# Optimization experiments

Hardware: AMD Instinct MI355X
Metric: run time of the kernel (lower is better)

The kernel has to match this reference:

```python
import jax, jax.numpy as jnp
import numpy as np

D, H, F, N, V, B, S, T = 512, 8, 2048, 2, 32000, 2, 1024, 1024


def _pe(seq_len, d):
    pos = np.arange(seq_len)[:, None].astype(np.float32)
    div = np.exp(np.arange(0, d, 2).astype(np.float32) * (-np.log(10000.0) / d))
    pe = np.zeros((seq_len, d), np.float32)
    pe[:, 0::2] = np.sin(pos * div)
    pe[:, 1::2] = np.cos(pos * div)
    return jnp.asarray(pe)


def _ln(x, g, b, eps=1e-6):
    # torch .var() default is unbiased (ddof=1)
    m = x.mean(-1, keepdims=True)
    v = jnp.sum((x - m) ** 2, -1, keepdims=True) / (x.shape[-1] - 1)
    return g * (x - m) / jnp.sqrt(v + eps) + b


def _mha(q, k, v, mask, w, b):
    # w: [4, D, D] (q,k,v,o); b: [4, D]
    Bq, Sq, Dm = q.shape
    Sk = k.shape[1]
    dk = Dm // H
    Q = (q @ w[0] + b[0]).reshape(Bq, Sq, H, dk).transpose(0, 2, 1, 3)
    K = (k @ w[1] + b[1]).reshape(Bq, Sk, H, dk).transpose(0, 2, 1, 3)
    Vv = (v @ w[2] + b[2]).reshape(Bq, Sk, H, dk).transpose(0, 2, 1, 3)
    s = jnp.einsum('bhqd,bhkd->bhqk', Q, K) / jnp.sqrt(jnp.float32(dk))
    s = jnp.where(mask == 0, jnp.float32(-1e9), s)
    a = jax.nn.softmax(s, axis=-1)
    o = jnp.einsum('bhqk,bhkd->bhqd', a, Vv).transpose(0, 2, 1, 3).reshape(Bq, Sq, Dm)
    return o @ w[3] + b[3]


def _ffn(x, w1, b1, w2, b2):
    return jax.nn.relu(x @ w1 + b1) @ w2 + b2


def _forward(src, tgt, src_mask, tgt_mask, p):
    (src_emb, tgt_emb, ea_w, ea_b, ef_w1, ef_b1, ef_w2, ef_b2, eln_g, eln_b, en_g, en_b,
     ds_w, ds_b, dc_w, dc_b, df_w1, df_b1, df_w2, df_b2, dln_g, dln_b, dn_g, dn_b, pw, pb) = p
    scale = jnp.sqrt(jnp.float32(D))
    # encoder
    x = src_emb[src] * scale + _pe(src.shape[1], D)
    for i in range(N):
        h = _ln(x, eln_g[i, 0], eln_b[i, 0])
        x = x + _mha(h, h, h, src_mask, ea_w[i], ea_b[i])
        h = _ln(x, eln_g[i, 1], eln_b[i, 1])
        x = x + _ffn(h, ef_w1[i], ef_b1[i], ef_w2[i], ef_b2[i])
    enc = _ln(x, en_g, en_b)
    # decoder
    y = tgt_emb[tgt] * scale + _pe(tgt.shape[1], D)
    for i in range(N):
        h = _ln(y, dln_g[i, 0], dln_b[i, 0])
        y = y + _mha(h, h, h, tgt_mask, ds_w[i], ds_b[i])
        h = _ln(y, dln_g[i, 1], dln_b[i, 1])
        y = y + _mha(h, enc, enc, src_mask, dc_w[i], dc_b[i])
        h = _ln(y, dln_g[i, 2], dln_b[i, 2])
        y = y + _ffn(h, df_w1[i], df_b1[i], df_w2[i], df_b2[i])
    y = _ln(y, dn_g, dn_b)
    return jax.nn.log_softmax(y @ pw + pb, axis=-1)


def setup_inputs() -> dict:
    key = jax.random.key(0)
    c = [0]
    def nk():
        c[0] += 1
        return jax.random.fold_in(key, c[0])
    def w(*s):
        return jax.random.normal(nk(), s, jnp.float32) * 0.02
    inp = {
        'src': jax.random.randint(nk(), (B, S), 0, V, jnp.int32),
        'tgt': jax.random.randint(nk(), (B, T), 0, V, jnp.int32),
        'src_mask': jnp.ones((B, 1, 1, S), jnp.int32),
        'tgt_mask': jnp.tril(jnp.ones((T, T), jnp.int32))[None, None],
        'src_emb': w(V, D), 'tgt_emb': w(V, D),
        'enc_attn_w': w(N, 4, D, D), 'enc_attn_b': jnp.zeros((N, 4, D), jnp.float32),
        'enc_ffn_w1': w(N, D, F), 'enc_ffn_b1': jnp.zeros((N, F), jnp.float32),
        'enc_ffn_w2': w(N, F, D), 'enc_ffn_b2': jnp.zeros((N, D), jnp.float32),
        'enc_ln_g': jnp.ones((N, 2, D), jnp.float32), 'enc_ln_b': jnp.zeros((N, 2, D), jnp.float32),
        'enc_norm_g': jnp.ones((D,), jnp.float32), 'enc_norm_b': jnp.zeros((D,), jnp.float32),
        'dec_self_w': w(N, 4, D, D), 'dec_self_b': jnp.zeros((N, 4, D), jnp.float32),
        'dec_cross_w': w(N, 4, D, D), 'dec_cross_b': jnp.zeros((N, 4, D), jnp.float32),
        'dec_ffn_w1': w(N, D, F), 'dec_ffn_b1': jnp.zeros((N, F), jnp.float32),
        'dec_ffn_w2': w(N, F, D), 'dec_ffn_b2': jnp.zeros((N, D), jnp.float32),
        'dec_ln_g': jnp.ones((N, 3, D), jnp.float32), 'dec_ln_b': jnp.zeros((N, 3, D), jnp.float32),
        'dec_norm_g': jnp.ones((D,), jnp.float32), 'dec_norm_b': jnp.zeros((D,), jnp.float32),
        'proj_w': w(D, V), 'proj_b': jnp.zeros((V,), jnp.float32),
    }
    return inp


def reference(src, tgt, src_mask, tgt_mask, src_emb, tgt_emb, enc_attn_w, enc_attn_b,
              enc_ffn_w1, enc_ffn_b1, enc_ffn_w2, enc_ffn_b2, enc_ln_g, enc_ln_b,
              enc_norm_g, enc_norm_b, dec_self_w, dec_self_b, dec_cross_w, dec_cross_b,
              dec_ffn_w1, dec_ffn_b1, dec_ffn_w2, dec_ffn_b2, dec_ln_g, dec_ln_b,
              dec_norm_g, dec_norm_b, proj_w, proj_b):
    p = (src_emb, tgt_emb, enc_attn_w, enc_attn_b, enc_ffn_w1, enc_ffn_b1, enc_ffn_w2,
         enc_ffn_b2, enc_ln_g, enc_ln_b, enc_norm_g, enc_norm_b, dec_self_w, dec_self_b,
         dec_cross_w, dec_cross_b, dec_ffn_w1, dec_ffn_b1, dec_ffn_w2, dec_ffn_b2,
         dec_ln_g, dec_ln_b, dec_norm_g, dec_norm_b, proj_w, proj_b)
    return _forward(src, tgt, src_mask, tgt_mask, p)
```

## Files before the change

kernel.cpp:

```cpp
#include <hip/hip_runtime.h>
#include <hip/hip_bf16.h>
#include <math.h>

using bf16 = __hip_bfloat16;
typedef float f32x4 __attribute__((ext_vector_type(4)));
typedef short short8 __attribute__((ext_vector_type(8)));

constexpr int kD = 512, kH = 8, kDk = 64, kF = 2048, kV = 32000;
constexpr int kB = 2, kS = 1024, kM = 2048, kBH = 16;

enum { ST_F32 = 0, ST_BF16, ST_QKV };

__device__ __forceinline__ void gload_lds16(const void* g, void* l) {
  __builtin_amdgcn_global_load_lds(
      (const __attribute__((address_space(1))) void*)g,
      (__attribute__((address_space(3))) void*)l, 16, 0, 0);
}

__device__ __forceinline__ float bfu2f(short u) {
  union { unsigned int i; float f; } c;
  c.i = ((unsigned int)(unsigned short)u) << 16;
  return c.f;
}

template <int BM, int BN, int STM, bool BIAS, bool RELU, bool RES, int NBUF, bool XSWZ, bool ASEL>
__launch_bounds__(256)
__global__ void k_gemm(const bf16* __restrict__ A, int lda, long long Az,
                       const bf16* __restrict__ Bt, int ldb, long long Bz,
                       void* __restrict__ Cv, int ldc, long long Cz,
                       int K, float alpha,
                       const float* __restrict__ bias,
                       const float* __restrict__ res,
                       const bf16* __restrict__ A2) {
  static_assert(NBUF == 1 || (BM == 64 && BN == 64), "pipeline path sized for 64x64");
  constexpr int FM = BM / 32, FN = BN / 32;
  __shared__ __attribute__((aligned(16))) bf16 As[NBUF][BM * 64];
  __shared__ __attribute__((aligned(16))) bf16 Bs[NBUF][BN * 64];
  const int tid = threadIdx.x;
  const int w = tid >> 6, lane = tid & 63;
  int bx = blockIdx.x, by = blockIdx.y;
  if constexpr (XSWZ) {
    const int nx = gridDim.x, ny = gridDim.y;
    const int lin = by * nx + bx;
    const int cpx = (nx * ny) >> 3;
    const int s = (lin & 7) * cpx + (lin >> 3);
    bx = s / ny;
    by = s - bx * ny;
  }
  const int bm = by * BM, bn = bx * BN;
  const int z = blockIdx.z;
  if constexpr (ASEL) { if (bn >= 512) A = A2; }
  A += (long long)z * Az;
  Bt += (long long)z * Bz;
  const int l15 = lane & 15, lhi = lane >> 4;
  const int wr = (w >> 1) * (BM / 2), wc = (w & 1) * (BN / 2);
  f32x4 acc[FM][FN] = {};
  const int nkt = K >> 6;

  auto stage = [&](int kt, int nb) {
#pragma unroll
    for (int it = 0; it < BM / 32; ++it) {
      int chunk = (it * 4 + w) * 64 + lane;
      int row = chunk >> 3, col = (chunk & 7) << 3;
      gload_lds16(A + (size_t)(bm + row) * lda + kt * 64 + col, As[nb] + (it * 4 + w) * 512);
    }
#pragma unroll
    for (int it = 0; it < BN / 32; ++it) {
      int chunk = (it * 4 + w) * 64 + lane;
      int row = chunk >> 3, col = (chunk & 7) << 3;
      gload_lds16(Bt + (size_t)(bn + row) * ldb + kt * 64 + col, Bs[nb] + (it * 4 + w) * 512);
    }
  };
  auto compute = [&](int cb) {
#pragma unroll
    for (int kk = 0; kk < 2; ++kk) {
      short8 af[FM], bf[FN];
#pragma unroll
      for (int i = 0; i < FM; ++i)
        af[i] = *(const short8*)(As[cb] + (wr + i * 16 + l15) * 64 + kk * 32 + lhi * 8);
#pragma unroll
      for (int j = 0; j < FN; ++j)
        bf[j] = *(const short8*)(Bs[cb] + (wc + j * 16 + l15) * 64 + kk * 32 + lhi * 8);
#pragma unroll
      for (int i = 0; i < FM; ++i)
#pragma unroll
        for (int j = 0; j < FN; ++j)
          acc[i][j] = __builtin_amdgcn_mfma_f32_16x16x32_bf16(af[i], bf[j], acc[i][j], 0, 0, 0);
    }
  };

  if constexpr (NBUF == 3) {
    stage(0, 0);
    stage(1, 1);
    stage(2, 2);
    asm volatile("s_waitcnt vmcnt(8)" ::: "memory");
    __builtin_amdgcn_s_barrier();
    __builtin_amdgcn_sched_barrier(0);
    int cur = 0;
    for (int kt = 0; kt < nkt; ++kt) {
      compute(cur);
      asm volatile("s_waitcnt lgkmcnt(0)" ::: "memory");
      __builtin_amdgcn_sched_barrier(0);
      if (kt + 1 < nkt) {
        __builtin_amdgcn_s_barrier();
        if (kt + 3 < nkt) {
          stage(kt + 3, cur);
          asm volatile("s_waitcnt vmcnt(8)" ::: "memory");
        } else {
          asm volatile("s_waitcnt vmcnt(0)" ::: "memory");
        }
        __builtin_amdgcn_s_barrier();
        __builtin_amdgcn_sched_barrier(0);
      }
      cur = (cur == 2) ? 0 : cur + 1;
    }
  } else {
    for (int kt = 0; kt < nkt; ++kt) {
      stage(kt, 0);
      __syncthreads();
      compute(0);
      __syncthreads();
    }
  }

#pragma unroll
  for (int i = 0; i < FM; ++i) {
#pragma unroll
    for (int j = 0; j < FN; ++j) {
#pragma unroll
      for (int r = 0; r < 4; ++r) {
        int m = bm + wr + i * 16 + lhi * 4 + r;
        int n = bn + wc + j * 16 + l15;
        float val = acc[i][j][r] * alpha;
        if constexpr (BIAS) val += bias[n];
        if constexpr (RELU) val = fmaxf(val, 0.f);
        if constexpr (RES) val += res[(size_t)m * ldc + n];
        if constexpr (STM == ST_F32) {
          ((float*)Cv)[(size_t)z * Cz + (size_t)m * ldc + n] = val;
        } else if constexpr (STM == ST_BF16) {
          ((bf16*)Cv)[(size_t)z * Cz + (size_t)m * ldc + n] = __float2bfloat16(val);
        } else if constexpr (STM == ST_QKV) {
          int seg = n >> 9, nn = n & 511;
          int b_ = m >> 10, s_ = m & 1023, h_ = nn >> 6, d_ = nn & 63;
          size_t idx = (seg < 2)
              ? (((size_t)(b_ * kH + h_) << 10) + s_) * kDk + d_
              : ((size_t)(b_ * kH + h_) * kDk + d_) * kS + s_;
          ((bf16*)Cv)[(size_t)seg * 1048576 + idx] = __float2bfloat16(val);
        }
      }
    }
  }
}

__global__ __launch_bounds__(512, 1) void k_proj256(const bf16* __restrict__ A,
                                                    const bf16* __restrict__ Bt,
                                                    bf16* __restrict__ C,
                                                    const float* __restrict__ bias) {
  __shared__ __attribute__((aligned(16))) bf16 As[4][256 * 32];
  __shared__ __attribute__((aligned(16))) bf16 Bs[4][256 * 32];
  const int tid = threadIdx.x, w = tid >> 6, lane = tid & 63;
  const int l15 = lane & 15, lhi = lane >> 4;
  const int lin = blockIdx.y * 125 + blockIdx.x;
  const int s = (lin & 7) * 125 + (lin >> 3);
  const int bx = s >> 3, by = s & 7;
  const int bm = by * 256, bn = bx * 256;
  const int wr = (w >> 2) * 128, wc = (w & 3) * 64;
  const int rowq = tid >> 2, chk = tid & 3;
  const int swz = (chk ^ ((rowq >> 1) & 3)) << 3;
  const bf16* Asrc0 = A + (size_t)(bm + rowq) * kD + swz;
  const bf16* Asrc1 = A + (size_t)(bm + 128 + rowq) * kD + swz;
  const bf16* Bsrc0 = Bt + (size_t)(bn + rowq) * kD + swz;
  const bf16* Bsrc1 = Bt + (size_t)(bn + 128 + rowq) * kD + swz;
  const int ldsoff = w * 1024;

  auto stage = [&](int kt) {
    const int b = kt & 3;
    const int ko = kt * 32;
    gload_lds16(Asrc0 + ko, (char*)As[b] + ldsoff);
    gload_lds16(Asrc1 + ko, (char*)As[b] + 8192 + ldsoff);
    gload_lds16(Bsrc0 + ko, (char*)Bs[b] + ldsoff);
    gload_lds16(Bsrc1 + ko, (char*)Bs[b] + 8192 + ldsoff);
  };

  const int ra = wr + l15, rb = wc + l15;
  const int abase = ra * 64 + ((lhi ^ ((ra >> 1) & 3)) << 4);
  const int bbase = rb * 64 + ((lhi ^ ((rb >> 1) & 3)) << 4);

  f32x4 acc[8][4] = {};
  stage(0); stage(1); stage(2);
  for (int kt = 0; kt < 16; ++kt) {
    if (kt + 2 < 16)      asm volatile("s_waitcnt vmcnt(8)" ::: "memory");
    else if (kt + 1 < 16) asm volatile("s_waitcnt vmcnt(4)" ::: "memory");
    else                  asm volatile("s_waitcnt vmcnt(0)" ::: "memory");
    __builtin_amdgcn_s_barrier();
    __builtin_amdgcn_sched_barrier(0);
    if (kt + 3 < 16) stage(kt + 3);
    const int b = kt & 3;
    short8 af[8], bf[4];
#pragma unroll
    for (int i = 0; i < 8; ++i)
      af[i] = *(const short8*)((const char*)As[b] + abase + i * 1024);
#pragma unroll
    for (int j = 0; j < 4; ++j)
      bf[j] = *(const short8*)((const char*)Bs[b] + bbase + j * 1024);
#pragma unroll
    for (int i = 0; i < 8; ++i)
#pragma unroll
      for (int j = 0; j < 4; ++j)
        acc[i][j] = __builtin_amdgcn_mfma_f32_16x16x32_bf16(af[i], bf[j], acc[i][j], 0, 0, 0);
    asm volatile("s_waitcnt lgkmcnt(0)" ::: "memory");
    __builtin_amdgcn_sched_barrier(0);
  }
#pragma unroll
  for (int i = 0; i < 8; ++i)
#pragma unroll
    for (int j = 0; j < 4; ++j)
#pragma unroll
      for (int r = 0; r < 4; ++r) {
        int m = bm + wr + i * 16 + lhi * 4 + r;
        int n = bn + wc + j * 16 + l15;
        C[(size_t)m * kV + n] = __float2bfloat16(acc[i][j][r] + bias[n]);
      }
}

template <bool CAUSAL>
__launch_bounds__(256)
__global__ void k_fattn(const bf16* __restrict__ Q, const bf16* __restrict__ K,
                        const bf16* __restrict__ Vt, bf16* __restrict__ O) {
  __shared__ __attribute__((aligned(16))) bf16 Ks[3][4096];
  __shared__ __attribute__((aligned(16))) bf16 Vs[3][4096];
  __shared__ __attribute__((aligned(16))) bf16 Ps[4][1024];
  const int tid = threadIdx.x, w = tid >> 6, lane = tid & 63;
  const int l15 = lane & 15, lhi = lane >> 4;
  const int q0 = blockIdx.x * 64, bh = blockIdx.y;
  const int qw = q0 + w * 16;
  const bf16* Qp = Q + (((size_t)(bh << 10)) + qw + l15) * kDk;
  short8 aq[2];
  aq[0] = *(const short8*)(Qp + lhi * 8);
  aq[1] = *(const short8*)(Qp + 32 + lhi * 8);
  const int srow = w * 8 + (lane >> 3);
  const int sc = (lane & 7) ^ (srow & 7);
  const bf16* Ksrc = K + (((size_t)(bh << 10)) + srow) * kDk + sc * 8;
  const bf16* Vsrc = Vt + ((size_t)bh * kDk + srow) * kS + sc * 8;
  const int nt = CAUSAL ? (q0 >> 6) + 1 : (kS >> 6);

  auto stage = [&](int t, int nb) {
    int kv0 = t << 6;
    gload_lds16(Ksrc + (size_t)kv0 * kDk, Ks[nb] + w * 512);
    gload_lds16(Ksrc + (size_t)(kv0 + 32) * kDk, Ks[nb] + 2048 + w * 512);
    gload_lds16(Vsrc + kv0, Vs[nb] + w * 512);
    gload_lds16(Vsrc + kv0 + 32 * kS, Vs[nb] + 2048 + w * 512);
  };

  float m_[4], l_[4];
#pragma unroll
  for (int r = 0; r < 4; ++r) { m_[r] = -1e30f; l_[r] = 0.f; }
  f32x4 ao[4] = {};

  stage(0, 0);
  if (nt > 2) {
    stage(1, 1);
    stage(2, 2);
    asm volatile("s_waitcnt vmcnt(8)" ::: "memory");
  } else if (nt > 1) {
    stage(1, 1);
    asm volatile("s_waitcnt vmcnt(4)" ::: "memory");
  } else {
    asm volatile("s_waitcnt vmcnt(0)" ::: "memory");
  }
  __builtin_amdgcn_s_barrier();
  __builtin_amdgcn_sched_barrier(0);

  int cur = 0;
  for (int t = 0; t < nt; ++t) {
    f32x4 as[4] = {};
#pragma unroll
    for (int kk = 0; kk < 2; ++kk) {
      short8 bk[4];
#pragma unroll
      for (int nf = 0; nf < 4; ++nf) {
        int row = nf * 16 + l15;
        int c = (4 * kk + lhi) ^ (row & 7);
        bk[nf] = *(const short8*)(Ks[cur] + row * 64 + c * 8);
      }
#pragma unroll
      for (int nf = 0; nf < 4; ++nf)
        as[nf] = __builtin_amdgcn_mfma_f32_16x16x32_bf16(aq[kk], bk[nf], as[nf], 0, 0, 0);
    }
    float s[4][4];
#pragma unroll
    for (int nf = 0; nf < 4; ++nf)
#pragma unroll
      for (int r = 0; r < 4; ++r) {
        float v = as[nf][r] * 0.125f;
        if (CAUSAL && t == nt - 1) {
          int col = (t << 6) + nf * 16 + l15;
          int row = qw + lhi * 4 + r;
          if (col > row) v = -1e30f;
        }
        s[nf][r] = v;
      }
    float mn[4], scl[4], rsum[4];
#pragma unroll
    for (int r = 0; r < 4; ++r) {
      float mx = fmaxf(fmaxf(s[0][r], s[1][r]), fmaxf(s[2][r], s[3][r]));
      mx = fmaxf(mx, __shfl_xor(mx, 1));
      mx = fmaxf(mx, __shfl_xor(mx, 2));
      mx = fmaxf(mx, __shfl_xor(mx, 4));
      mx = fmaxf(mx, __shfl_xor(mx, 8));
      mn[r] = fmaxf(m_[r], mx);
      scl[r] = __expf(m_[r] - mn[r]);
      rsum[r] = 0.f;
    }
#pragma unroll
    for (int nf = 0; nf < 4; ++nf)
#pragma unroll
      for (int r = 0; r < 4; ++r) {
        float p = __expf(s[nf][r] - mn[r]);
        rsum[r] += p;
        int pr = lhi * 4 + r;
        int c = (2 * nf + (l15 >> 3)) ^ (pr & 7);
        Ps[w][pr * 64 + c * 8 + (l15 & 7)] = __float2bfloat16(p);
      }
#pragma unroll
    for (int r = 0; r < 4; ++r) {
      float su = rsum[r];
      su += __shfl_xor(su, 1);
      su += __shfl_xor(su, 2);
      su += __shfl_xor(su, 4);
      su += __shfl_xor(su, 8);
      l_[r] = l_[r] * scl[r] + su;
      m_[r] = mn[r];
    }
#pragma unroll
    for (int nf = 0; nf < 4; ++nf)
#pragma unroll
      for (int r = 0; r < 4; ++r) ao[nf][r] *= scl[r];
    asm volatile("s_waitcnt lgkmcnt(0)" ::: "memory");
    __builtin_amdgcn_sched_barrier(0);
#pragma unroll
    for (int kk = 0; kk < 2; ++kk) {
      short8 pa = *(const short8*)(Ps[w] + l15 * 64 + (((4 * kk + lhi) ^ (l15 & 7)) * 8));
      short8 bv[4];
#pragma unroll
      for (int nf = 0; nf < 4; ++nf) {
        int row = nf * 16 + l15;
        int c = (4 * kk + lhi) ^ (row & 7);
        bv[nf] = *(const short8*)(Vs[cur] + row * 64 + c * 8);
      }
#pragma unroll
      for (int nf = 0; nf < 4; ++nf)
        ao[nf] = __builtin_amdgcn_mfma_f32_16x16x32_bf16(pa, bv[nf], ao[nf], 0, 0, 0);
    }
    asm volatile("s_waitcnt lgkmcnt(0)" ::: "memory");
    __builtin_amdgcn_sched_barrier(0);
    if (t + 1 < nt) {
      __builtin_amdgcn_s_barrier();
      if (t + 3 < nt) {
        stage(t + 3, cur);
        asm volatile("s_waitcnt vmcnt(8)" ::: "memory");
      } else {
        asm volatile("s_waitcnt vmcnt(0)" ::: "memory");
      }
      __builtin_amdgcn_s_barrier();
      __builtin_amdgcn_sched_barrier(0);
    }
    cur = (cur == 2) ? 0 : cur + 1;
  }
  const int b_ = bh >> 3, h_ = bh & 7;
  float inv[4];
#pragma unroll
  for (int r = 0; r < 4; ++r) inv[r] = 1.f / l_[r];
#pragma unroll
  for (int nf = 0; nf < 4; ++nf)
#pragma unroll
    for (int r = 0; r < 4; ++r) {
      int q = qw + lhi * 4 + r;
      O[((size_t)(b_ * kS + q)) * kD + h_ * kDk + nf * 16 + l15] =
          __float2bfloat16(ao[nf][r] * inv[r]);
    }
}

struct TJobs {
  const float* src[8];
  bf16* dst[8];
  int K[8], N[8];
  int ofs[9];
};

__global__ void k_transpose_all(TJobs J) {
  __shared__ float t[32][33];
  const int tb = blockIdx.x;
  int j = 0;
#pragma unroll
  for (int i = 1; i < 8; ++i) j += (tb >= J.ofs[i]) ? 1 : 0;
  const int K = J.K[j], N = J.N[j];
  const int tn = N >> 5, tk = K >> 5;
  int r = tb - J.ofs[j];
  const int z = r / (tn * tk);
  r -= z * tn * tk;
  const int k0 = (r / tn) << 5, n0 = (r % tn) << 5;
  const float* Wp = J.src[j] + (size_t)z * K * N;
  bf16* WTp = J.dst[j] + (size_t)z * K * N;
  const int tx = threadIdx.x, ty = threadIdx.y;
#pragma unroll
  for (int rr = 0; rr < 32; rr += 8) t[ty + rr][tx] = Wp[(size_t)(k0 + ty + rr) * N + n0 + tx];
  __syncthreads();
#pragma unroll
  for (int rr = 0; rr < 32; rr += 8)
    WTp[(size_t)(n0 + ty + rr) * K + k0 + tx] = __float2bfloat16(t[tx][ty + rr]);
}

__global__ void k_embed2(const int* __restrict__ src, const int* __restrict__ tgt,
                         const float* __restrict__ se, const float* __restrict__ te,
                         float* __restrict__ xe, float* __restrict__ xd) {
  const int m = blockIdx.x, which = blockIdx.y;
  const int* tok = which ? tgt : src;
  const float* emb = which ? te : se;
  float* x = which ? xd : xe;
  int s = m & (kS - 1);
  const float* e = emb + (size_t)tok[m] * kD;
  float* xp = x + (size_t)m * kD;
  for (int d = threadIdx.x; d < kD; d += 256) {
    int i = d >> 1;
    float freq = __expf(-(float)(2 * i) * (9.210340371976184f / 512.0f));
    float ang = (float)s * freq;
    float pe = (d & 1) ? cosf(ang) : sinf(ang);
    xp[d] = e[d] * 22.62741699796952f + pe;
  }
}

__global__ void k_ln(const float* __restrict__ x, const float* __restrict__ g,
                     const float* __restrict__ b, bf16* __restrict__ out) {
  int w = threadIdx.x >> 6, lane = threadIdx.x & 63;
  int row = blockIdx.x * 4 + w;
  const float* xp = x + (size_t)row * kD;
  float v[8];
  float sum = 0.f;
#pragma unroll
  for (int i = 0; i < 8; ++i) { v[i] = xp[lane + i * 64]; sum += v[i]; }
#pragma unroll
  for (int o = 32; o; o >>= 1) sum += __shfl_xor(sum, o);
  float mean = sum * (1.f / 512.f);
  float sq = 0.f;
#pragma unroll
  for (int i = 0; i < 8; ++i) { float d = v[i] - mean; sq += d * d; }
#pragma unroll
  for (int o = 32; o; o >>= 1) sq += __shfl_xor(sq, o);
  float inv = rsqrtf(sq * (1.f / 511.f) + 1e-6f);
  bf16* op = out + (size_t)row * kD;
#pragma unroll
  for (int i = 0; i < 8; ++i) {
    int d = lane + i * 64;
    op[d] = __float2bfloat16(g[d] * (v[i] - mean) * inv + b[d]);
  }
}

__global__ __launch_bounds__(640, 2) void k_lsm_bf(const bf16* __restrict__ L,
                                                   float* __restrict__ y) {
  const bf16* row = L + (size_t)blockIdx.x * kV;
  float* orow = y + (size_t)blockIdx.x * kV;
  const int t = threadIdx.x;
  const bool extra = t < 160;
  float v[56];
  float sum = 0.f;
#pragma unroll
  for (int i = 0; i < 6; ++i) {
    short8 s = *(const short8*)(row + (t + i * 640) * 8);
#pragma unroll
    for (int e = 0; e < 8; ++e) {
      float f = bfu2f(s[e]);
      v[i * 8 + e] = f;
      sum += __expf(f);
    }
  }
  if (extra) {
    short8 s = *(const short8*)(row + (3840 + t) * 8);
#pragma unroll
    for (int e = 0; e < 8; ++e) {
      float f = bfu2f(s[e]);
      v[48 + e] = f;
      sum += __expf(f);
    }
  }
#pragma unroll
  for (int o = 32; o; o >>= 1) sum += __shfl_xor(sum, o);
  __shared__ float red2[10];
  const int w = t >> 6, lane = t & 63;
  if (lane == 0) red2[w] = sum;
  __syncthreads();
  sum = 0.f;
#pragma unroll
  for (int i = 0; i < 10; ++i) sum += red2[i];
  const float sh = logf(sum);
#pragma unroll
  for (int i = 0; i < 6; ++i)
#pragma unroll
    for (int e = 0; e < 8; ++e) orow[(t + i * 640) * 8 + e] = v[i * 8 + e] - sh;
  if (extra)
#pragma unroll
    for (int e = 0; e < 8; ++e) orow[(3840 + t) * 8 + e] = v[48 + e] - sh;
}

extern "C" void kernel_launch(void* const* d_in, const int* in_sizes, int n_in,
                              void* d_out, int out_size, void* d_ws, size_t ws_size,
                              hipStream_t stream) {
  (void)in_sizes; (void)n_in; (void)out_size;
  if (ws_size < (size_t)212 * 1024 * 1024) return;

  const int* src = (const int*)d_in[0];
  const int* tgt = (const int*)d_in[1];
  const float* src_emb   = (const float*)d_in[4];
  const float* tgt_emb   = (const float*)d_in[5];
  const float* enc_attn_w = (const float*)d_in[6];
  const float* enc_attn_b = (const float*)d_in[7];
  const float* enc_ffn_w1 = (const float*)d_in[8];
  const float* enc_ffn_b1 = (const float*)d_in[9];
  const float* enc_ffn_w2 = (const float*)d_in[10];
  const float* enc_ffn_b2 = (const float*)d_in[11];
  const float* enc_ln_g  = (const float*)d_in[12];
  const float* enc_ln_b  = (const float*)d_in[13];
  const float* enc_norm_g = (const float*)d_in[14];
  const float* enc_norm_b = (const float*)d_in[15];
  const float* dec_self_w = (const float*)d_in[16];
  const float* dec_self_b = (const float*)d_in[17];
  const float* dec_cross_w = (const float*)d_in[18];
  const float* dec_cross_b = (const float*)d_in[19];
  const float* dec_ffn_w1 = (const float*)d_in[20];
  const float* dec_ffn_b1 = (const float*)d_in[21];
  const float* dec_ffn_w2 = (const float*)d_in[22];
  const float* dec_ffn_b2 = (const float*)d_in[23];
  const float* dec_ln_g  = (const float*)d_in[24];
  const float* dec_ln_b  = (const float*)d_in[25];
  const float* dec_norm_g = (const float*)d_in[26];
  const float* dec_norm_b = (const float*)d_in[27];
  const float* proj_w    = (const float*)d_in[28];
  const float* proj_b    = (const float*)d_in[29];

  char* ws = (char*)d_ws;
  auto MB = [](size_t x) { return x << 20; };
  bf16* enc_attn_wt  = (bf16*)(ws + MB(0));
  bf16* dec_self_wt  = (bf16*)(ws + MB(4));
  bf16* dec_cross_wt = (bf16*)(ws + MB(8));
  bf16* enc_f1t = (bf16*)(ws + MB(12));
  bf16* enc_f2t = (bf16*)(ws + MB(16));
  bf16* dec_f1t = (bf16*)(ws + MB(20));
  bf16* dec_f2t = (bf16*)(ws + MB(24));
  bf16* proj_wt = (bf16*)(ws + MB(28));
  float* x_enc  = (float*)(ws + MB(60));
  float* x_dec  = (float*)(ws + MB(64));
  bf16* hbuf    = (bf16*)(ws + MB(68));
  bf16* enc_bf  = (bf16*)(ws + MB(70));
  bf16* Qb      = (bf16*)(ws + MB(72));
  bf16* attn_o  = (bf16*)(ws + MB(78));
  bf16* logits  = (bf16*)(ws + MB(80));
  bf16* ffn_mid = (bf16*)d_out;

  TJobs tj;
  int acc = 0;
  auto setj = [&](int j, const float* s, bf16* d, int K, int N, int z) {
    tj.src[j] = s; tj.dst[j] = d; tj.K[j] = K; tj.N[j] = N; tj.ofs[j] = acc;
    acc += (K >> 5) * (N >> 5) * z;
  };
  setj(0, enc_attn_w, enc_attn_wt, 512, 512, 8);
  setj(1, dec_self_w, dec_self_wt, 512, 512, 8);
  setj(2, dec_cross_w, dec_cross_wt, 512, 512, 8);
  setj(3, enc_ffn_w1, enc_f1t, 512, 2048, 2);
  setj(4, enc_ffn_w2, enc_f2t, 2048, 512, 2);
  setj(5, dec_ffn_w1, dec_f1t, 512, 2048, 2);
  setj(6, dec_ffn_w2, dec_f2t, 2048, 512, 2);
  setj(7, proj_w, proj_wt, 512, 32000, 1);
  tj.ofs[8] = acc;
  k_transpose_all<<<acc, dim3(32, 8), 0, stream>>>(tj);

  k_embed2<<<dim3(kM, 2), 256, 0, stream>>>(src, tgt, src_emb, tgt_emb, x_enc, x_dec);

  auto LN = [&](const float* x, const float* g, const float* b, bf16* out) {
    k_ln<<<kM / 4, 256, 0, stream>>>(x, g, b, out);
  };
  auto out_proj = [&](const bf16* wt, const float* bias, float* xio) {
    k_gemm<64, 64, ST_F32, true, false, true, 3, false, false><<<dim3(8, 32, 1), 256, 0, stream>>>(
        attn_o, 512, 0, wt + 3 * 262144, 512, 0, xio, 512, 0, 512, 1.f, bias + 3 * 512, xio, nullptr);
  };
  auto self_attn = [&](const bf16* wt, const float* bias, bool causal, float* xio) {
    k_gemm<64, 64, ST_QKV, true, false, false, 3, false, false><<<dim3(24, 32, 1), 256, 0, stream>>>(
        hbuf, 512, 0, wt, 512, 0, Qb, 0, 0, 512, 1.f, bias, nullptr, nullptr);
    if (causal) k_fattn<true><<<dim3(16, kBH), 256, 0, stream>>>(Qb, Qb + 1048576, Qb + 2097152, attn_o);
    else        k_fattn<false><<<dim3(16, kBH), 256, 0, stream>>>(Qb, Qb + 1048576, Qb + 2097152, attn_o);
    out_proj(wt, bias, xio);
  };
  auto cross_attn = [&](const bf16* wt, const float* bias, float* xio) {
    k_gemm<64, 64, ST_QKV, true, false, false, 3, false, true><<<dim3(24, 32, 1), 256, 0, stream>>>(
        hbuf, 512, 0, wt, 512, 0, Qb, 0, 0, 512, 1.f, bias, nullptr, enc_bf);
    k_fattn<false><<<dim3(16, kBH), 256, 0, stream>>>(Qb, Qb + 1048576, Qb + 2097152, attn_o);
    out_proj(wt, bias, xio);
  };
  auto ffn_block = [&](float* xio, const bf16* w1t, const float* b1, const bf16* w2t,
                       const float* b2, const float* g, const float* bl) {
    LN(xio, g, bl, hbuf);
    k_gemm<64, 64, ST_BF16, true, true, false, 3, false, false><<<dim3(32, 32, 1), 256, 0, stream>>>(
        hbuf, 512, 0, w1t, 512, 0, ffn_mid, kF, 0, 512, 1.f, b1, nullptr, nullptr);
    k_gemm<64, 64, ST_F32, true, false, true, 3, false, false><<<dim3(8, 32, 1), 256, 0, stream>>>(
        ffn_mid, 2048, 0, w2t, 2048, 0, xio, 512, 0, 2048, 1.f, b2, xio, nullptr);
  };

  for (int i = 0; i < 2; ++i) {
    LN(x_enc, enc_ln_g + i * 1024, enc_ln_b + i * 1024, hbuf);
    self_attn(enc_attn_wt + (size_t)i * 1048576, enc_attn_b + i * 2048, false, x_enc);
    ffn_block(x_enc, enc_f1t + (size_t)i * 1048576, enc_ffn_b1 + i * 2048,
              enc_f2t + (size_t)i * 1048576, enc_ffn_b2 + i * 512,
              enc_ln_g + i * 1024 + 512, enc_ln_b + i * 1024 + 512);
  }
  LN(x_enc, enc_norm_g, enc_norm_b, enc_bf);

  for (int i = 0; i < 2; ++i) {
    LN(x_dec, dec_ln_g + i * 1536, dec_ln_b + i * 1536, hbuf);
    self_attn(dec_self_wt + (size_t)i * 1048576, dec_self_b + i * 2048, true, x_dec);
    LN(x_dec, dec_ln_g + i * 1536 + 512, dec_ln_b + i * 1536 + 512, hbuf);
    cross_attn(dec_cross_wt + (size_t)i * 1048576, dec_cross_b + i * 2048, x_dec);
    ffn_block(x_dec, dec_f1t + (size_t)i * 1048576, dec_ffn_b1 + i * 2048,
              dec_f2t + (size_t)i * 1048576, dec_ffn_b2 + i * 512,
              dec_ln_g + i * 1536 + 1024, dec_ln_b + i * 1536 + 1024);
  }
  LN(x_dec, dec_norm_g, dec_norm_b, hbuf);

  k_proj256<<<dim3(125, 8), 512, 0, stream>>>(hbuf, proj_wt, logits, proj_b);
  k_lsm_bf<<<kM, 640, 0, stream>>>(logits, (float*)d_out);
}
```

Measured before the change: 726.8 us.

## Fuse encoder/decoder layer kernels into a persistent megakernel with grid barriers

Replaces the sequence of many small kernel launches (transpose, embed, layernorm, QKV GEMM, attention, out-proj, FFN GEMMs) with one persistent 256-block kernel. Phases are separated by a software grid barrier built on atomics, and each block loops over virtual tiles. The aim is to remove launch overhead and inter-kernel gaps between dozens of short kernels. In exchange, occupancy is fixed at one 256-thread block per CU, some phases such as attention (256 tiles) or FFN1 (1024 tiles) may balance poorly, and each grid barrier adds its own spin-wait cost.

```diff
diff --git a/kernel.cpp b/kernel.cpp
--- a/kernel.cpp
+++ b/kernel.cpp
@@ -8,6 +8,7 @@
 
 constexpr int kD = 512, kH = 8, kDk = 64, kF = 2048, kV = 32000;
 constexpr int kB = 2, kS = 1024, kM = 2048, kBH = 16;
+constexpr unsigned kGrid = 256;
 
 enum { ST_F32 = 0, ST_BF16, ST_QKV };
 
@@ -23,122 +24,204 @@
   return c.f;
 }
 
-template <int BM, int BN, int STM, bool BIAS, bool RELU, bool RES, int NBUF, bool XSWZ, bool ASEL>
-__launch_bounds__(256)
-__global__ void k_gemm(const bf16* __restrict__ A, int lda, long long Az,
-                       const bf16* __restrict__ Bt, int ldb, long long Bz,
-                       void* __restrict__ Cv, int ldc, long long Cz,
-                       int K, float alpha,
-                       const float* __restrict__ bias,
-                       const float* __restrict__ res,
-                       const bf16* __restrict__ A2) {
-  static_assert(NBUF == 1 || (BM == 64 && BN == 64), "pipeline path sized for 64x64");
-  constexpr int FM = BM / 32, FN = BN / 32;
-  __shared__ __attribute__((aligned(16))) bf16 As[NBUF][BM * 64];
-  __shared__ __attribute__((aligned(16))) bf16 Bs[NBUF][BN * 64];
-  const int tid = threadIdx.x;
-  const int w = tid >> 6, lane = tid & 63;
-  int bx = blockIdx.x, by = blockIdx.y;
-  if constexpr (XSWZ) {
-    const int nx = gridDim.x, ny = gridDim.y;
-    const int lin = by * nx + bx;
-    const int cpx = (nx * ny) >> 3;
-    const int s = (lin & 7) * cpx + (lin >> 3);
-    bx = s / ny;
-    by = s - bx * ny;
-  }
-  const int bm = by * BM, bn = bx * BN;
-  const int z = blockIdx.z;
-  if constexpr (ASEL) { if (bn >= 512) A = A2; }
-  A += (long long)z * Az;
-  Bt += (long long)z * Bz;
+__device__ __forceinline__ void gbar(unsigned* bar, unsigned* gen) {
+  __threadfence();
+  __syncthreads();
+  if (threadIdx.x == 0) {
+    unsigned g = __hip_atomic_load(gen, __ATOMIC_RELAXED, __HIP_MEMORY_SCOPE_AGENT);
+    unsigned v = __hip_atomic_fetch_add(bar, 1u, __ATOMIC_ACQ_REL, __HIP_MEMORY_SCOPE_AGENT);
+    if (v == kGrid - 1u) {
+      __hip_atomic_store(bar, 0u, __ATOMIC_RELAXED, __HIP_MEMORY_SCOPE_AGENT);
+      __hip_atomic_store(gen, g + 1u, __ATOMIC_RELEASE, __HIP_MEMORY_SCOPE_AGENT);
+    } else {
+      while (__hip_atomic_load(gen, __ATOMIC_ACQUIRE, __HIP_MEMORY_SCOPE_AGENT) == g)
+        __builtin_amdgcn_s_sleep(2);
+    }
+  }
+  __syncthreads();
+}
+
+struct TJobs {
+  const float* src[8];
+  bf16* dst[8];
+  int K[8], N[8];
+  int ofs[9];
+};
+
+struct MegaArgs {
+  const int* src; const int* tgt;
+  const float* src_emb; const float* tgt_emb;
+  float* x_enc; float* x_dec;
+  TJobs tj; int ntile;
+  unsigned *bar, *gen;
+  bf16 *hbuf, *enc_bf, *Qb, *attn_o, *ffn_mid;
+  const bf16 *enc_attn_wt, *dec_self_wt, *dec_cross_wt;
+  const bf16 *enc_f1t, *enc_f2t, *dec_f1t, *dec_f2t;
+  const float *enc_attn_b, *enc_ffn_b1, *enc_ffn_b2, *enc_ln_g, *enc_ln_b;
+  const float *enc_norm_g, *enc_norm_b;
+  const float *dec_self_b, *dec_cross_b, *dec_ffn_b1, *dec_ffn_b2;
+  const float *dec_ln_g, *dec_ln_b, *dec_norm_g, *dec_norm_b;
+};
+
+
+__device__ __forceinline__ void transpose_tile(char* smemc, int tb, const TJobs& J) {
+  float (*t)[33] = (float (*)[33])smemc;
+  int j = 0;
+#pragma unroll
+  for (int i = 1; i < 8; ++i) j += (tb >= J.ofs[i]) ? 1 : 0;
+  const int K = J.K[j], N = J.N[j];
+  const int tn = N >> 5, tk = K >> 5;
+  int r = tb - J.ofs[j];
+  const int z = r / (tn * tk);
+  r -= z * tn * tk;
+  const int k0 = (r / tn) << 5, n0 = (r % tn) << 5;
+  const float* Wp = J.src[j] + (size_t)z * K * N;
+  bf16* WTp = J.dst[j] + (size_t)z * K * N;
+  const int tx = threadIdx.x & 31, ty = threadIdx.x >> 5;
+#pragma unroll
+  for (int rr = 0; rr < 32; rr += 8) t[ty + rr][tx] = Wp[(size_t)(k0 + ty + rr) * N + n0 + tx];
+  __syncthreads();
+#pragma unroll
+  for (int rr = 0; rr < 32; rr += 8)
+    WTp[(size_t)(n0 + ty + rr) * K + k0 + tx] = __float2bfloat16(t[tx][ty + rr]);
+  __syncthreads();
+}
+
+__device__ __forceinline__ void embed_row(int vb, const MegaArgs& a) {
+  const int m = vb & (kM - 1), which = vb >> 11;
+  const int* tok = which ? a.tgt : a.src;
+  const float* emb = which ? a.tgt_emb : a.src_emb;
+  float* x = which ? a.x_dec : a.x_enc;
+  int s = m & (kS - 1);
+  const float* e = emb + (size_t)tok[m] * kD;
+  float* xp = x + (size_t)m * kD;
+  for (int d = threadIdx.x; d < kD; d += 256) {
+    int i = d >> 1;
+    float freq = __expf(-(float)(2 * i) * (9.210340371976184f / 512.0f));
+    float ang = (float)s * freq;
+    float pe = (d & 1) ? cosf(ang) : sinf(ang);
+    xp[d] = e[d] * 22.62741699796952f + pe;
+  }
+}
+
+__device__ __forceinline__ void ln4(int vb, const float* __restrict__ x,
+                                    const float* __restrict__ g,
+                                    const float* __restrict__ b,
+                                    bf16* __restrict__ out) {
+  int w = threadIdx.x >> 6, lane = threadIdx.x & 63;
+  int row = vb * 4 + w;
+  const float* xp = x + (size_t)row * kD;
+  float v[8];
+  float sum = 0.f;
+#pragma unroll
+  for (int i = 0; i < 8; ++i) { v[i] = xp[lane + i * 64]; sum += v[i]; }
+#pragma unroll
+  for (int o = 32; o; o >>= 1) sum += __shfl_xor(sum, o);
+  float mean = sum * (1.f / 512.f);
+  float sq = 0.f;
+#pragma unroll
+  for (int i = 0; i < 8; ++i) { float d = v[i] - mean; sq += d * d; }
+#pragma unroll
+  for (int o = 32; o; o >>= 1) sq += __shfl_xor(sq, o);
+  float inv = rsqrtf(sq * (1.f / 511.f) + 1e-6f);
+  bf16* op = out + (size_t)row * kD;
+#pragma unroll
+  for (int i = 0; i < 8; ++i) {
+    int d = lane + i * 64;
+    op[d] = __float2bfloat16(g[d] * (v[i] - mean) * inv + b[d]);
+  }
+}
+
+template <int STM, bool BIAS, bool RELU, bool RES>
+__device__ __forceinline__ void gemm64_tile(
+    bf16* AsB, bf16* BsB, int bm, int bn,
+    const bf16* __restrict__ A, int lda,
+    const bf16* __restrict__ Bt, int ldb,
+    void* __restrict__ Cv, int ldc, int K,
+    const float* __restrict__ bias, const float* __restrict__ res) {
+  const int tid = threadIdx.x, w = tid >> 6, lane = tid & 63;
   const int l15 = lane & 15, lhi = lane >> 4;
-  const int wr = (w >> 1) * (BM / 2), wc = (w & 1) * (BN / 2);
-  f32x4 acc[FM][FN] = {};
+  const int wr = (w >> 1) * 32, wc = (w & 1) * 32;
+  f32x4 acc[2][2] = {};
   const int nkt = K >> 6;
 
   auto stage = [&](int kt, int nb) {
-#pragma unroll
-    for (int it = 0; it < BM / 32; ++it) {
+    bf16* As = AsB + nb * 4096;
+    bf16* Bs = BsB + nb * 4096;
+#pragma unroll
+    for (int it = 0; it < 2; ++it) {
       int chunk = (it * 4 + w) * 64 + lane;
       int row = chunk >> 3, col = (chunk & 7) << 3;
-      gload_lds16(A + (size_t)(bm + row) * lda + kt * 64 + col, As[nb] + (it * 4 + w) * 512);
-    }
-#pragma unroll
-    for (int it = 0; it < BN / 32; ++it) {
+      gload_lds16(A + (size_t)(bm + row) * lda + kt * 64 + col, As + (it * 4 + w) * 512);
+    }
+#pragma unroll
+    for (int it = 0; it < 2; ++it) {
       int chunk = (it * 4 + w) * 64 + lane;
       int row = chunk >> 3, col = (chunk & 7) << 3;
-      gload_lds16(Bt + (size_t)(bn + row) * ldb + kt * 64 + col, Bs[nb] + (it * 4 + w) * 512);
+      gload_lds16(Bt + (size_t)(bn + row) * ldb + kt * 64 + col, Bs + (it * 4 + w) * 512);
     }
   };
   auto compute = [&](int cb) {
+    bf16* As = AsB + cb * 4096;
+    bf16* Bs = BsB + cb * 4096;
 #pragma unroll
     for (int kk = 0; kk < 2; ++kk) {
-      short8 af[FM], bf[FN];
-#pragma unroll
-      for (int i = 0; i < FM; ++i)
-        af[i] = *(const short8*)(As[cb] + (wr + i * 16 + l15) * 64 + kk * 32 + lhi * 8);
-#pragma unroll
-      for (int j = 0; j < FN; ++j)
-        bf[j] = *(const short8*)(Bs[cb] + (wc + j * 16 + l15) * 64 + kk * 32 + lhi * 8);
-#pragma unroll
-      for (int i = 0; i < FM; ++i)
-#pragma unroll
-        for (int j = 0; j < FN; ++j)
+      short8 af[2], bf[2];
+#pragma unroll
+      for (int i = 0; i < 2; ++i)
+        af[i] = *(const short8*)(As + (wr + i * 16 + l15) * 64 + kk * 32 + lhi * 8);
+#pragma unroll
+      for (int j = 0; j < 2; ++j)
+        bf[j] = *(const short8*)(Bs + (wc + j * 16 + l15) * 64 + kk * 32 + lhi * 8);
+#pragma unroll
+      for (int i = 0; i < 2; ++i)
+#pragma unroll
+        for (int j = 0; j < 2; ++j)
           acc[i][j] = __builtin_amdgcn_mfma_f32_16x16x32_bf16(af[i], bf[j], acc[i][j], 0, 0, 0);
     }
   };
 
-  if constexpr (NBUF == 3) {
-    stage(0, 0);
-    stage(1, 1);
-    stage(2, 2);
-    asm volatile("s_waitcnt vmcnt(8)" ::: "memory");
-    __builtin_amdgcn_s_barrier();
+  stage(0, 0); stage(1, 1); stage(2, 2);
+  asm volatile("s_waitcnt vmcnt(8)" ::: "memory");
+  __builtin_amdgcn_s_barrier();
+  __builtin_amdgcn_sched_barrier(0);
+  int cur = 0;
+  for (int kt = 0; kt < nkt; ++kt) {
+    compute(cur);
+    asm volatile("s_waitcnt lgkmcnt(0)" ::: "memory");
     __builtin_amdgcn_sched_barrier(0);
-    int cur = 0;
-    for (int kt = 0; kt < nkt; ++kt) {
-      compute(cur);
-      asm volatile("s_waitcnt lgkmcnt(0)" ::: "memory");
+    if (kt + 1 < nkt) {
+      __builtin_amdgcn_s_barrier();
+      if (kt + 3 < nkt) {
+        stage(kt + 3, cur);
+        asm volatile("s_waitcnt vmcnt(8)" ::: "memory");
+      } else {
+        asm volatile("s_waitcnt vmcnt(0)" ::: "memory");
+      }
+      __builtin_amdgcn_s_barrier();
       __builtin_amdgcn_sched_barrier(0);
-      if (kt + 1 < nkt) {
-        __builtin_amdgcn_s_barrier();
-        if (kt + 3 < nkt) {
-          stage(kt + 3, cur);
-          asm volatile("s_waitcnt vmcnt(8)" ::: "memory");
-        } else {
-          asm volatile("s_waitcnt vmcnt(0)" ::: "memory");
-        }
-        __builtin_amdgcn_s_barrier();
-        __builtin_amdgcn_sched_barrier(0);
-      }
-      cur = (cur == 2) ? 0 : cur + 1;
-    }
-  } else {
-    for (int kt = 0; kt < nkt; ++kt) {
-      stage(kt, 0);
-      __syncthreads();
-      compute(0);
-      __syncthreads();
-    }
-  }
-
-#pragma unroll
-  for (int i = 0; i < FM; ++i) {
-#pragma unroll
-    for (int j = 0; j < FN; ++j) {
+    }
+    cur = (cur == 2) ? 0 : cur + 1;
+  }
+  __builtin_amdgcn_s_barrier();
+  __builtin_amdgcn_sched_barrier(0);
+
+#pragma unroll
+  for (int i = 0; i < 2; ++i) {
+#pragma unroll
+    for (int j = 0; j < 2; ++j) {
 #pragma unroll
       for (int r = 0; r < 4; ++r) {
         int m = bm + wr + i * 16 + lhi * 4 + r;
         int n = bn + wc + j * 16 + l15;
-        float val = acc[i][j][r] * alpha;
+        float val = acc[i][j][r];
         if constexpr (BIAS) val += bias[n];
         if constexpr (RELU) val = fmaxf(val, 0.f);
         if constexpr (RES) val += res[(size_t)m * ldc + n];
         if constexpr (STM == ST_F32) {
-          ((float*)Cv)[(size_t)z * Cz + (size_t)m * ldc + n] = val;
+          ((float*)Cv)[(size_t)m * ldc + n] = val;
         } else if constexpr (STM == ST_BF16) {
-          ((bf16*)Cv)[(size_t)z * Cz + (size_t)m * ldc + n] = __float2bfloat16(val);
+          ((bf16*)Cv)[(size_t)m * ldc + n] = __float2bfloat16(val);
         } else if constexpr (STM == ST_QKV) {
           int seg = n >> 9, nn = n & 511;
           int b_ = m >> 10, s_ = m & 1023, h_ = nn >> 6, d_ = nn & 63;
@@ -150,6 +233,255 @@
       }
     }
   }
+}
+
+template <bool CAUSAL>
+__device__ __forceinline__ void fattn_tile(bf16* Ks, bf16* Vs, bf16* Ps,
+                                           int qi, int bh,
+                                           const bf16* __restrict__ Q,
+                                           const bf16* __restrict__ K,
+                                           const bf16* __restrict__ Vt,
+                                           bf16* __restrict__ O) {
+  const int tid = threadIdx.x, w = tid >> 6, lane = tid & 63;
+  const int l15 = lane & 15, lhi = lane >> 4;
+  const int q0 = qi * 64;
+  const int qw = q0 + w * 16;
+  const bf16* Qp = Q + (((size_t)(bh << 10)) + qw + l15) * kDk;
+  short8 aq[2];
+  aq[0] = *(const short8*)(Qp + lhi * 8);
+  aq[1] = *(const short8*)(Qp + 32 + lhi * 8);
+  const int srow = w * 8 + (lane >> 3);
+  const int sc = (lane & 7) ^ (srow & 7);
+  const bf16* Ksrc = K + (((size_t)(bh << 10)) + srow) * kDk + sc * 8;
+  const bf16* Vsrc = Vt + ((size_t)bh * kDk + srow) * kS + sc * 8;
+  const int nt = CAUSAL ? (q0 >> 6) + 1 : (kS >> 6);
+
+  auto stage = [&](int t, int nb) {
+    int kv0 = t << 6;
+    gload_lds16(Ksrc + (size_t)kv0 * kDk, Ks + nb * 4096 + w * 512);
+    gload_lds16(Ksrc + (size_t)(kv0 + 32) * kDk, Ks + nb * 4096 + 2048 + w * 512);
+    gload_lds16(Vsrc + kv0, Vs + nb * 4096 + w * 512);
+    gload_lds16(Vsrc + kv0 + 32 * kS, Vs + nb * 4096 + 2048 + w * 512);
+  };
+
+  float m_[4], l_[4];
+#pragma unroll
+  for (int r = 0; r < 4; ++r) { m_[r] = -1e30f; l_[r] = 0.f; }
+  f32x4 ao[4] = {};
+
+  stage(0, 0);
+  if (nt > 2) {
+    stage(1, 1);
+    stage(2, 2);
+    asm volatile("s_waitcnt vmcnt(8)" ::: "memory");
+  } else if (nt > 1) {
+    stage(1, 1);
+    asm volatile("s_waitcnt vmcnt(4)" ::: "memory");
+  } else {
+    asm volatile("s_waitcnt vmcnt(0)" ::: "memory");
+  }
+  __builtin_amdgcn_s_barrier();
+  __builtin_amdgcn_sched_barrier(0);
+
+  int cur = 0;
+  for (int t = 0; t < nt; ++t) {
+    f32x4 as[4] = {};
+#pragma unroll
+    for (int kk = 0; kk < 2; ++kk) {
+      short8 bk[4];
+#pragma unroll
+      for (int nf = 0; nf < 4; ++nf) {
+        int row = nf * 16 + l15;
+        int c = (4 * kk + lhi) ^ (row & 7);
+        bk[nf] = *(const short8*)(Ks + cur * 4096 + row * 64 + c * 8);
+      }
+#pragma unroll
+      for (int nf = 0; nf < 4; ++nf)
+        as[nf] = __builtin_amdgcn_mfma_f32_16x16x32_bf16(aq[kk], bk[nf], as[nf], 0, 0, 0);
+    }
+    float s[4][4];
+#pragma unroll
+    for (int nf = 0; nf < 4; ++nf)
+#pragma unroll
+      for (int r = 0; r < 4; ++r) {
+        float v = as[nf][r] * 0.125f;
+        if (CAUSAL && t == nt - 1) {
+          int col = (t << 6) + nf * 16 + l15;
+          int row = qw + lhi * 4 + r;
+          if (col > row) v = -1e30f;
+        }
+        s[nf][r] = v;
+      }
+    float mn[4], scl[4], rsum[4];
+#pragma unroll
+    for (int r = 0; r < 4; ++r) {
+      float mx = fmaxf(fmaxf(s[0][r], s[1][r]), fmaxf(s[2][r], s[3][r]));
+      mx = fmaxf(mx, __shfl_xor(mx, 1));
+      mx = fmaxf(mx, __shfl_xor(mx, 2));
+      mx = fmaxf(mx, __shfl_xor(mx, 4));
+      mx = fmaxf(mx, __shfl_xor(mx, 8));
+      mn[r] = fmaxf(m_[r], mx);
+      scl[r] = __expf(m_[r] - mn[r]);
+      rsum[r] = 0.f;
+    }
+#pragma unroll
+    for (int nf = 0; nf < 4; ++nf)
+#pragma unroll
+      for (int r = 0; r < 4; ++r) {
+        float p = __expf(s[nf][r] - mn[r]);
+        rsum[r] += p;
+        int pr = lhi * 4 + r;
+        int c = (2 * nf + (l15 >> 3)) ^ (pr & 7);
+        Ps[w * 1024 + pr * 64 + c * 8 + (l15 & 7)] = __float2bfloat16(p);
+      }
+#pragma unroll
+    for (int r = 0; r < 4; ++r) {
+      float su = rsum[r];
+      su += __shfl_xor(su, 1);
+      su += __shfl_xor(su, 2);
+      su += __shfl_xor(su, 4);
+      su += __shfl_xor(su, 8);
+      l_[r] = l_[r] * scl[r] + su;
+      m_[r] = mn[r];
+    }
+#pragma unroll
+    for (int nf = 0; nf < 4; ++nf)
+#pragma unroll
+      for (int r = 0; r < 4; ++r) ao[nf][r] *= scl[r];
+    asm volatile("s_waitcnt lgkmcnt(0)" ::: "memory");
+    __builtin_amdgcn_sched_barrier(0);
+#pragma unroll
+    for (int kk = 0; kk < 2; ++kk) {
+      short8 pa = *(const short8*)(Ps + w * 1024 + l15 * 64 + (((4 * kk + lhi) ^ (l15 & 7)) * 8));
+      short8 bv[4];
+#pragma unroll
+      for (int nf = 0; nf < 4; ++nf) {
+        int row = nf * 16 + l15;
+        int c = (4 * kk + lhi) ^ (row & 7);
+        bv[nf] = *(const short8*)(Vs + cur * 4096 + row * 64 + c * 8);
+      }
+#pragma unroll
+      for (int nf = 0; nf < 4; ++nf)
+        ao[nf] = __builtin_amdgcn_mfma_f32_16x16x32_bf16(pa, bv[nf], ao[nf], 0, 0, 0);
+    }
+    asm volatile("s_waitcnt lgkmcnt(0)" ::: "memory");
+    __builtin_amdgcn_sched_barrier(0);
+    if (t + 1 < nt) {
+      __builtin_amdgcn_s_barrier();
+      if (t + 3 < nt) {
+        stage(t + 3, cur);
+        asm volatile("s_waitcnt vmcnt(8)" ::: "memory");
+      } else {
+        asm volatile("s_waitcnt vmcnt(0)" ::: "memory");
+      }
+      __builtin_amdgcn_s_barrier();
+      __builtin_amdgcn_sched_barrier(0);
+    }
+    cur = (cur == 2) ? 0 : cur + 1;
+  }
+  const int b_ = bh >> 3, h_ = bh & 7;
+  float inv[4];
+#pragma unroll
+  for (int r = 0; r < 4; ++r) inv[r] = 1.f / l_[r];
+#pragma unroll
+  for (int nf = 0; nf < 4; ++nf)
+#pragma unroll
+    for (int r = 0; r < 4; ++r) {
+      int q = qw + lhi * 4 + r;
+      O[((size_t)(b_ * kS + q)) * kD + h_ * kDk + nf * 16 + l15] =
+          __float2bfloat16(ao[nf][r] * inv[r]);
+    }
+}
+
+__global__ void __launch_bounds__(256, 1) k_mega(MegaArgs a) {
+  __shared__ __attribute__((aligned(16))) char smem[57344];
+  bf16* S0 = (bf16*)smem;
+  bf16* S1 = (bf16*)(smem + 24576);
+  bf16* S2 = (bf16*)(smem + 49152);
+  const int bid = blockIdx.x;
+
+  auto SYNC = [&]() { gbar(a.bar, a.gen); };
+
+  for (int vb = bid; vb < a.ntile; vb += 256) transpose_tile(smem, vb, a.tj);
+  for (int vb = bid; vb < 2 * kM; vb += 256) embed_row(vb, a);
+  SYNC();
+
+  auto LN_PH = [&](const float* x, const float* g, const float* b, bf16* out) {
+    for (int vb = bid; vb < 512; vb += 256) ln4(vb, x, g, b, out);
+    SYNC();
+  };
+  auto QKV_PH = [&](const bf16* wt, const float* bias, const bf16* kvA) {
+    for (int vb = bid; vb < 768; vb += 256) {
+      int bx = vb % 24, by = vb / 24;
+      int bn = bx * 64, bm = by * 64;
+      const bf16* Ause = (kvA != nullptr && bn >= 512) ? kvA : a.hbuf;
+      gemm64_tile<ST_QKV, true, false, false>(S0, S1, bm, bn, Ause, 512, wt, 512,
+                                              a.Qb, 0, 512, bias, nullptr);
+    }
+    SYNC();
+  };
+  auto ATTN_PH = [&](bool causal) {
+    int qi = bid & 15, bh = bid >> 4;
+    if (causal)
+      fattn_tile<true>(S0, S1, S2, qi, bh, a.Qb, a.Qb + 1048576, a.Qb + 2097152, a.attn_o);
+    else
+      fattn_tile<false>(S0, S1, S2, qi, bh, a.Qb, a.Qb + 1048576, a.Qb + 2097152, a.attn_o);
+    SYNC();
+  };
+  auto OUTPROJ_PH = [&](const bf16* wt, const float* bias, float* xio) {
+    int bx = bid & 7, by = bid >> 3;
+    gemm64_tile<ST_F32, true, false, true>(S0, S1, by * 64, bx * 64, a.attn_o, 512,
+                                           wt + 3 * 262144, 512, xio, 512, 512,
+                                           bias + 3 * 512, xio);
+    SYNC();
+  };
+  auto FFN1_PH = [&](const bf16* w1t, const float* b1) {
+    for (int vb = bid; vb < 1024; vb += 256) {
+      int bx = vb & 31, by = vb >> 5;
+      gemm64_tile<ST_BF16, true, true, false>(S0, S1, by * 64, bx * 64, a.hbuf, 512,
+                                              w1t, 512, a.ffn_mid, kF, 512, b1, nullptr);
+    }
+    SYNC();
+  };
+  auto FFN2_PH = [&](const bf16* w2t, const float* b2, float* xio) {
+    int bx = bid & 7, by = bid >> 3;
+    gemm64_tile<ST_F32, true, false, true>(S0, S1, by * 64, bx * 64, a.ffn_mid, kF,
+                                           w2t, kF, xio, 512, kF, b2, xio);
+    SYNC();
+  };
+
+  for (int i = 0; i < 2; ++i) {
+    const bf16* wt = a.enc_attn_wt + (size_t)i * 1048576;
+    const float* bias = a.enc_attn_b + i * 2048;
+    LN_PH(a.x_enc, a.enc_ln_g + i * 1024, a.enc_ln_b + i * 1024, a.hbuf);
+    QKV_PH(wt, bias, nullptr);
+    ATTN_PH(false);
+    OUTPROJ_PH(wt, bias, a.x_enc);
+    LN_PH(a.x_enc, a.enc_ln_g + i * 1024 + 512, a.enc_ln_b + i * 1024 + 512, a.hbuf);
+    FFN1_PH(a.enc_f1t + (size_t)i * 1048576, a.enc_ffn_b1 + i * 2048);
+    FFN2_PH(a.enc_f2t + (size_t)i * 1048576, a.enc_ffn_b2 + i * 512, a.x_enc);
+  }
+  LN_PH(a.x_enc, a.enc_norm_g, a.enc_norm_b, a.enc_bf);
+
+  for (int i = 0; i < 2; ++i) {
+    const bf16* wts = a.dec_self_wt + (size_t)i * 1048576;
+    const float* bs = a.dec_self_b + i * 2048;
+    const bf16* wtc = a.dec_cross_wt + (size_t)i * 1048576;
+    const float* bc = a.dec_cross_b + i * 2048;
+    LN_PH(a.x_dec, a.dec_ln_g + i * 1536, a.dec_ln_b + i * 1536, a.hbuf);
+    QKV_PH(wts, bs, nullptr);
+    ATTN_PH(true);
+    OUTPROJ_PH(wts, bs, a.x_dec);
+    LN_PH(a.x_dec, a.dec_ln_g + i * 1536 + 512, a.dec_ln_b + i * 1536 + 512, a.hbuf);
+    QKV_PH(wtc, bc, a.enc_bf);
+    ATTN_PH(false);
+    OUTPROJ_PH(wtc, bc, a.x_dec);
+    LN_PH(a.x_dec, a.dec_ln_g + i * 1536 + 1024, a.dec_ln_b + i * 1536 + 1024, a.hbuf);
+    FFN1_PH(a.dec_f1t + (size_t)i * 1048576, a.dec_ffn_b1 + i * 2048);
+    FFN2_PH(a.dec_f2t + (size_t)i * 1048576, a.dec_ffn_b2 + i * 512, a.x_dec);
+  }
+  for (int vb = bid; vb < 512; vb += 256)
+    ln4(vb, a.x_dec, a.dec_norm_g, a.dec_norm_b, a.hbuf);
 }
 
 __global__ __launch_bounds__(512, 1) void k_proj256(const bf16* __restrict__ A,
@@ -223,239 +555,6 @@
       }
 }
 
-template <bool CAUSAL>
-__launch_bounds__(256)
-__global__ void k_fattn(const bf16* __restrict__ Q, const bf16* __restrict__ K,
-                        const bf16* __restrict__ Vt, bf16* __restrict__ O) {
-  __shared__ __attribute__((aligned(16))) bf16 Ks[3][4096];
-  __shared__ __attribute__((aligned(16))) bf16 Vs[3][4096];
-  __shared__ __attribute__((aligned(16))) bf16 Ps[4][1024];
-  const int tid = threadIdx.x, w = tid >> 6, lane = tid & 63;
-  const int l15 = lane & 15, lhi = lane >> 4;
-  const int q0 = blockIdx.x * 64, bh = blockIdx.y;
-  const int qw = q0 + w * 16;
-  const bf16* Qp = Q + (((size_t)(bh << 10)) + qw + l15) * kDk;
-  short8 aq[2];
-  aq[0] = *(const short8*)(Qp + lhi * 8);
-  aq[1] = *(const short8*)(Qp + 32 + lhi * 8);
-  const int srow = w * 8 + (lane >> 3);
-  const int sc = (lane & 7) ^ (srow & 7);
-  const bf16* Ksrc = K + (((size_t)(bh << 10)) + srow) * kDk + sc * 8;
-  const bf16* Vsrc = Vt + ((size_t)bh * kDk + srow) * kS + sc * 8;
-  const int nt = CAUSAL ? (q0 >> 6) + 1 : (kS >> 6);
-
-  auto stage = [&](int t, int nb) {
-    int kv0 = t << 6;
-    gload_lds16(Ksrc + (size_t)kv0 * kDk, Ks[nb] + w * 512);
-    gload_lds16(Ksrc + (size_t)(kv0 + 32) * kDk, Ks[nb] + 2048 + w * 512);
-    gload_lds16(Vsrc + kv0, Vs[nb] + w * 512);
-    gload_lds16(Vsrc + kv0 + 32 * kS, Vs[nb] + 2048 + w * 512);
-  };
-
-  float m_[4], l_[4];
-#pragma unroll
-  for (int r = 0; r < 4; ++r) { m_[r] = -1e30f; l_[r] = 0.f; }
-  f32x4 ao[4] = {};
-
-  stage(0, 0);
-  if (nt > 2) {
-    stage(1, 1);
-    stage(2, 2);
-    asm volatile("s_waitcnt vmcnt(8)" ::: "memory");
-  } else if (nt > 1) {
-    stage(1, 1);
-    asm volatile("s_waitcnt vmcnt(4)" ::: "memory");
-  } else {
-    asm volatile("s_waitcnt vmcnt(0)" ::: "memory");
-  }
-  __builtin_amdgcn_s_barrier();
-  __builtin_amdgcn_sched_barrier(0);
-
-  int cur = 0;
-  for (int t = 0; t < nt; ++t) {
-    f32x4 as[4] = {};
-#pragma unroll
-    for (int kk = 0; kk < 2; ++kk) {
-      short8 bk[4];
-#pragma unroll
-      for (int nf = 0; nf < 4; ++nf) {
-        int row = nf * 16 + l15;
-        int c = (4 * kk + lhi) ^ (row & 7);
-        bk[nf] = *(const short8*)(Ks[cur] + row * 64 + c * 8);
-      }
-#pragma unroll
-      for (int nf = 0; nf < 4; ++nf)
-        as[nf] = __builtin_amdgcn_mfma_f32_16x16x32_bf16(aq[kk], bk[nf], as[nf], 0, 0, 0);
-    }
-    float s[4][4];
-#pragma unroll
-    for (int nf = 0; nf < 4; ++nf)
-#pragma unroll
-      for (int r = 0; r < 4; ++r) {
-        float v = as[nf][r] * 0.125f;
-        if (CAUSAL && t == nt - 1) {
-          int col = (t << 6) + nf * 16 + l15;
-          int row = qw + lhi * 4 + r;
-          if (col > row) v = -1e30f;
-        }
-        s[nf][r] = v;
-      }
-    float mn[4], scl[4], rsum[4];
-#pragma unroll
-    for (int r = 0; r < 4; ++r) {
-      float mx = fmaxf(fmaxf(s[0][r], s[1][r]), fmaxf(s[2][r], s[3][r]));
-      mx = fmaxf(mx, __shfl_xor(mx, 1));
-      mx = fmaxf(mx, __shfl_xor(mx, 2));
-      mx = fmaxf(mx, __shfl_xor(mx, 4));
-      mx = fmaxf(mx, __shfl_xor(mx, 8));
-      mn[r] = fmaxf(m_[r], mx);
-      scl[r] = __expf(m_[r] - mn[r]);
-      rsum[r] = 0.f;
-    }
-#pragma unroll
-    for (int nf = 0; nf < 4; ++nf)
-#pragma unroll
-      for (int r = 0; r < 4; ++r) {
-        float p = __expf(s[nf][r] - mn[r]);
-        rsum[r] += p;
-        int pr = lhi * 4 + r;
-        int c = (2 * nf + (l15 >> 3)) ^ (pr & 7);
-        Ps[w][pr * 64 + c * 8 + (l15 & 7)] = __float2bfloat16(p);
-      }
-#pragma unroll
-    for (int r = 0; r < 4; ++r) {
-      float su = rsum[r];
-      su += __shfl_xor(su, 1);
-      su += __shfl_xor(su, 2);
-      su += __shfl_xor(su, 4);
-      su += __shfl_xor(su, 8);
-      l_[r] = l_[r] * scl[r] + su;
-      m_[r] = mn[r];
-    }
-#pragma unroll
-    for (int nf = 0; nf < 4; ++nf)
-#pragma unroll
-      for (int r = 0; r < 4; ++r) ao[nf][r] *= scl[r];
-    asm volatile("s_waitcnt lgkmcnt(0)" ::: "memory");
-    __builtin_amdgcn_sched_barrier(0);
-#pragma unroll
-    for (int kk = 0; kk < 2; ++kk) {
-      short8 pa = *(const short8*)(Ps[w] + l15 * 64 + (((4 * kk + lhi) ^ (l15 & 7)) * 8));
-      short8 bv[4];
-#pragma unroll
-      for (int nf = 0; nf < 4; ++nf) {
-        int row = nf * 16 + l15;
-        int c = (4 * kk + lhi) ^ (row & 7);
-        bv[nf] = *(const short8*)(Vs[cur] + row * 64 + c * 8);
-      }
-#pragma unroll
-      for (int nf = 0; nf < 4; ++nf)
-        ao[nf] = __builtin_amdgcn_mfma_f32_16x16x32_bf16(pa, bv[nf], ao[nf], 0, 0, 0);
-    }
-    asm volatile("s_waitcnt lgkmcnt(0)" ::: "memory");
-    __builtin_amdgcn_sched_barrier(0);
-    if (t + 1 < nt) {
-      __builtin_amdgcn_s_barrier();
-      if (t + 3 < nt) {
-        stage(t + 3, cur);
-        asm volatile("s_waitcnt vmcnt(8)" ::: "memory");
-      } else {
-        asm volatile("s_waitcnt vmcnt(0)" ::: "memory");
-      }
-      __builtin_amdgcn_s_barrier();
-      __builtin_amdgcn_sched_barrier(0);
-    }
-    cur = (cur == 2) ? 0 : cur + 1;
-  }
-  const int b_ = bh >> 3, h_ = bh & 7;
-  float inv[4];
-#pragma unroll
-  for (int r = 0; r < 4; ++r) inv[r] = 1.f / l_[r];
-#pragma unroll
-  for (int nf = 0; nf < 4; ++nf)
-#pragma unroll
-    for (int r = 0; r < 4; ++r) {
-      int q = qw + lhi * 4 + r;
-      O[((size_t)(b_ * kS + q)) * kD + h_ * kDk + nf * 16 + l15] =
-          __float2bfloat16(ao[nf][r] * inv[r]);
-    }
-}
-
-struct TJobs {
-  const float* src[8];
-  bf16* dst[8];
-  int K[8], N[8];
-  int ofs[9];
-};
-
-__global__ void k_transpose_all(TJobs J) {
-  __shared__ float t[32][33];
-  const int tb = blockIdx.x;
-  int j = 0;
-#pragma unroll
-  for (int i = 1; i < 8; ++i) j += (tb >= J.ofs[i]) ? 1 : 0;
-  const int K = J.K[j], N = J.N[j];
-  const int tn = N >> 5, tk = K >> 5;
-  int r = tb - J.ofs[j];
-  const int z = r / (tn * tk);
-  r -= z * tn * tk;
-  const int k0 = (r / tn) << 5, n0 = (r % tn) << 5;
-  const float* Wp = J.src[j] + (size_t)z * K * N;
-  bf16* WTp = J.dst[j] + (size_t)z * K * N;
-  const int tx = threadIdx.x, ty = threadIdx.y;
-#pragma unroll
-  for (int rr = 0; rr < 32; rr += 8) t[ty + rr][tx] = Wp[(size_t)(k0 + ty + rr) * N + n0 + tx];
-  __syncthreads();
-#pragma unroll
-  for (int rr = 0; rr < 32; rr += 8)
-    WTp[(size_t)(n0 + ty + rr) * K + k0 + tx] = __float2bfloat16(t[tx][ty + rr]);
-}
-
-__global__ void k_embed2(const int* __restrict__ src, const int* __restrict__ tgt,
-                         const float* __restrict__ se, const float* __restrict__ te,
-                         float* __restrict__ xe, float* __restrict__ xd) {
-  const int m = blockIdx.x, which = blockIdx.y;
-  const int* tok = which ? tgt : src;
-  const float* emb = which ? te : se;
-  float* x = which ? xd : xe;
-  int s = m & (kS - 1);
-  const float* e = emb + (size_t)tok[m] * kD;
-  float* xp = x + (size_t)m * kD;
-  for (int d = threadIdx.x; d < kD; d += 256) {
-    int i = d >> 1;
-    float freq = __expf(-(float)(2 * i) * (9.210340371976184f / 512.0f));
-    float ang = (float)s * freq;
-    float pe = (d & 1) ? cosf(ang) : sinf(ang);
-    xp[d] = e[d] * 22.62741699796952f + pe;
-  }
-}
-
-__global__ void k_ln(const float* __restrict__ x, const float* __restrict__ g,
-                     const float* __restrict__ b, bf16* __restrict__ out) {
-  int w = threadIdx.x >> 6, lane = threadIdx.x & 63;
-  int row = blockIdx.x * 4 + w;
-  const float* xp = x + (size_t)row * kD;
-  float v[8];
-  float sum = 0.f;
-#pragma unroll
-  for (int i = 0; i < 8; ++i) { v[i] = xp[lane + i * 64]; sum += v[i]; }
-#pragma unroll
-  for (int o = 32; o; o >>= 1) sum += __shfl_xor(sum, o);
-  float mean = sum * (1.f / 512.f);
-  float sq = 0.f;
-#pragma unroll
-  for (int i = 0; i < 8; ++i) { float d = v[i] - mean; sq += d * d; }
-#pragma unroll
-  for (int o = 32; o; o >>= 1) sq += __shfl_xor(sq, o);
-  float inv = rsqrtf(sq * (1.f / 511.f) + 1e-6f);
-  bf16* op = out + (size_t)row * kD;
-#pragma unroll
-  for (int i = 0; i < 8; ++i) {
-    int d = lane + i * 64;
-    op[d] = __float2bfloat16(g[d] * (v[i] - mean) * inv + b[d]);
-  }
-}
-
 __global__ __launch_bounds__(640, 2) void k_lsm_bf(const bf16* __restrict__ L,
                                                    float* __restrict__ y) {
   const bf16* row = L + (size_t)blockIdx.x * kV;
@@ -508,37 +607,39 @@
   (void)in_sizes; (void)n_in; (void)out_size;
   if (ws_size < (size_t)212 * 1024 * 1024) return;
 
-  const int* src = (const int*)d_in[0];
-  const int* tgt = (const int*)d_in[1];
-  const float* src_emb   = (const float*)d_in[4];
-  const float* tgt_emb   = (const float*)d_in[5];
-  const float* enc_attn_w = (const float*)d_in[6];
-  const float* enc_attn_b = (const float*)d_in[7];
-  const float* enc_ffn_w1 = (const float*)d_in[8];
-  const float* enc_ffn_b1 = (const float*)d_in[9];
-  const float* enc_ffn_w2 = (const float*)d_in[10];
-  const float* enc_ffn_b2 = (const float*)d_in[11];
-  const float* enc_ln_g  = (const float*)d_in[12];
-  const float* enc_ln_b  = (const float*)d_in[13];
-  const float* enc_norm_g = (const float*)d_in[14];
-  const float* enc_norm_b = (const float*)d_in[15];
-  const float* dec_self_w = (const float*)d_in[16];
-  const float* dec_self_b = (const float*)d_in[17];
-  const float* dec_cross_w = (const float*)d_in[18];
-  const float* dec_cross_b = (const float*)d_in[19];
-  const float* dec_ffn_w1 = (const float*)d_in[20];
-  const float* dec_ffn_b1 = (const float*)d_in[21];
-  const float* dec_ffn_w2 = (const float*)d_in[22];
-  const float* dec_ffn_b2 = (const float*)d_in[23];
-  const float* dec_ln_g  = (const float*)d_in[24];
-  const float* dec_ln_b  = (const float*)d_in[25];
-  const float* dec_norm_g = (const float*)d_in[26];
-  const float* dec_norm_b = (const float*)d_in[27];
-  const float* proj_w    = (const float*)d_in[28];
-  const float* proj_b    = (const float*)d_in[29];
-
   char* ws = (char*)d_ws;
   auto MB = [](size_t x) { return x << 20; };
+
+  MegaArgs a;
+  a.src = (const int*)d_in[0];
+  a.tgt = (const int*)d_in[1];
+  a.src_emb = (const float*)d_in[4];
+  a.tgt_emb = (const float*)d_in[5];
+  const float* enc_attn_w = (const float*)d_in[6];
+  a.enc_attn_b = (const float*)d_in[7];
+  const float* enc_ffn_w1 = (const float*)d_in[8];
+  a.enc_ffn_b1 = (const float*)d_in[9];
+  const float* enc_ffn_w2 = (const float*)d_in[10];
+  a.enc_ffn_b2 = (const float*)d_in[11];
+  a.enc_ln_g = (const float*)d_in[12];
+  a.enc_ln_b = (const float*)d_in[13];
+  a.enc_norm_g = (const float*)d_in[14];
+  a.enc_norm_b = (const float*)d_in[15];
+  const float* dec_self_w = (const float*)d_in[16];
+  a.dec_self_b = (const float*)d_in[17];
+  const float* dec_cross_w = (const float*)d_in[18];
+  a.dec_cross_b = (const float*)d_in[19];
+  const float* dec_ffn_w1 = (const float*)d_in[20];
+  a.dec_ffn_b1 = (const float*)d_in[21];
+  const float* dec_ffn_w2 = (const float*)d_in[22];
+  a.dec_ffn_b2 = (const float*)d_in[23];
+  a.dec_ln_g = (const float*)d_in[24];
+  a.dec_ln_b = (const float*)d_in[25];
+  a.dec_norm_g = (const float*)d_in[26];
+  a.dec_norm_b = (const float*)d_in[27];
+  const float* proj_w = (const float*)d_in[28];
+  const float* proj_b = (const float*)d_in[29];
+
   bf16* enc_attn_wt  = (bf16*)(ws + MB(0));
   bf16* dec_self_wt  = (bf16*)(ws + MB(4));
   bf16* dec_cross_wt = (bf16*)(ws + MB(8));
@@ -547,19 +648,26 @@
   bf16* dec_f1t = (bf16*)(ws + MB(20));
   bf16* dec_f2t = (bf16*)(ws + MB(24));
   bf16* proj_wt = (bf16*)(ws + MB(28));
-  float* x_enc  = (float*)(ws + MB(60));
-  float* x_dec  = (float*)(ws + MB(64));
-  bf16* hbuf    = (bf16*)(ws + MB(68));
-  bf16* enc_bf  = (bf16*)(ws + MB(70));
-  bf16* Qb      = (bf16*)(ws + MB(72));
-  bf16* attn_o  = (bf16*)(ws + MB(78));
-  bf16* logits  = (bf16*)(ws + MB(80));
-  bf16* ffn_mid = (bf16*)d_out;
-
-  TJobs tj;
+  a.x_enc = (float*)(ws + MB(60));
+  a.x_dec = (float*)(ws + MB(64));
+  a.hbuf = (bf16*)(ws + MB(68));
+  a.enc_bf = (bf16*)(ws + MB(70));
+  a.Qb = (bf16*)(ws + MB(72));
+  a.attn_o = (bf16*)(ws + MB(78));
+  bf16* logits = (bf16*)(ws + MB(80));
+  unsigned* barmem = (unsigned*)(ws + MB(206));
+  a.ffn_mid = (bf16*)d_out;
+  a.bar = barmem;
+  a.gen = barmem + 64;
+  a.enc_attn_wt = enc_attn_wt;
+  a.dec_self_wt = dec_self_wt;
+  a.dec_cross_wt = dec_cross_wt;
+  a.enc_f1t = enc_f1t; a.enc_f2t = enc_f2t;
+  a.dec_f1t = dec_f1t; a.dec_f2t = dec_f2t;
+
   int acc = 0;
   auto setj = [&](int j, const float* s, bf16* d, int K, int N, int z) {
-    tj.src[j] = s; tj.dst[j] = d; tj.K[j] = K; tj.N[j] = N; tj.ofs[j] = acc;
+    a.tj.src[j] = s; a.tj.dst[j] = d; a.tj.K[j] = K; a.tj.N[j] = N; a.tj.ofs[j] = acc;
     acc += (K >> 5) * (N >> 5) * z;
   };
   setj(0, enc_attn_w, enc_attn_wt, 512, 512, 8);
@@ -570,60 +678,11 @@
   setj(5, dec_ffn_w1, dec_f1t, 512, 2048, 2);
   setj(6, dec_ffn_w2, dec_f2t, 2048, 512, 2);
   setj(7, proj_w, proj_wt, 512, 32000, 1);
-  tj.ofs[8] = acc;
-  k_transpose_all<<<acc, dim3(32, 8), 0, stream>>>(tj);
-
-  k_embed2<<<dim3(kM, 2), 256, 0, stream>>>(src, tgt, src_emb, tgt_emb, x_enc, x_dec);
-
-  auto LN = [&](const float* x, const float* g, const float* b, bf16* out) {
-    k_ln<<<kM / 4, 256, 0, stream>>>(x, g, b, out);
-  };
-  auto out_proj = [&](const bf16* wt, const float* bias, float* xio) {
-    k_gemm<64, 64, ST_F32, true, false, true, 3, false, false><<<dim3(8, 32, 1), 256, 0, stream>>>(
-        attn_o, 512, 0, wt + 3 * 262144, 512, 0, xio, 512, 0, 512, 1.f, bias + 3 * 512, xio, nullptr);
-  };
-  auto self_attn = [&](const bf16* wt, const float* bias, bool causal, float* xio) {
-    k_gemm<64, 64, ST_QKV, true, false, false, 3, false, false><<<dim3(24, 32, 1), 256, 0, stream>>>(
-        hbuf, 512, 0, wt, 512, 0, Qb, 0, 0, 512, 1.f, bias, nullptr, nullptr);
-    if (causal) k_fattn<true><<<dim3(16, kBH), 256, 0, stream>>>(Qb, Qb + 1048576, Qb + 2097152, attn_o);
-    else        k_fattn<false><<<dim3(16, kBH), 256, 0, stream>>>(Qb, Qb + 1048576, Qb + 2097152, attn_o);
-    out_proj(wt, bias, xio);
-  };
-  auto cross_attn = [&](const bf16* wt, const float* bias, float* xio) {
-    k_gemm<64, 64, ST_QKV, true, false, false, 3, false, true><<<dim3(24, 32, 1), 256, 0, stream>>>(
-        hbuf, 512, 0, wt, 512, 0, Qb, 0, 0, 512, 1.f, bias, nullptr, enc_bf);
-    k_fattn<false><<<dim3(16, kBH), 256, 0, stream>>>(Qb, Qb + 1048576, Qb + 2097152, attn_o);
-    out_proj(wt, bias, xio);
-  };
-  auto ffn_block = [&](float* xio, const bf16* w1t, const float* b1, const bf16* w2t,
-                       const float* b2, const float* g, const float* bl) {
-    LN(xio, g, bl, hbuf);
-    k_gemm<64, 64, ST_BF16, true, true, false, 3, false, false><<<dim3(32, 32, 1), 256, 0, stream>>>(
-        hbuf, 512, 0, w1t, 512, 0, ffn_mid, kF, 0, 512, 1.f, b1, nullptr, nullptr);
-    k_gemm<64, 64, ST_F32, true, false, true, 3, false, false><<<dim3(8, 32, 1), 256, 0, stream>>>(
-        ffn_mid, 2048, 0, w2t, 2048, 0, xio, 512, 0, 2048, 1.f, b2, xio, nullptr);
-  };
-
-  for (int i = 0; i < 2; ++i) {
-    LN(x_enc, enc_ln_g + i * 1024, enc_ln_b + i * 1024, hbuf);
-    self_attn(enc_attn_wt + (size_t)i * 1048576, enc_attn_b + i * 2048, false, x_enc);
-    ffn_block(x_enc, enc_f1t + (size_t)i * 1048576, enc_ffn_b1 + i * 2048,
-              enc_f2t + (size_t)i * 1048576, enc_ffn_b2 + i * 512,
-              enc_ln_g + i * 1024 + 512, enc_ln_b + i * 1024 + 512);
-  }
-  LN(x_enc, enc_norm_g, enc_norm_b, enc_bf);
-
-  for (int i = 0; i < 2; ++i) {
-    LN(x_dec, dec_ln_g + i * 1536, dec_ln_b + i * 1536, hbuf);
-    self_attn(dec_self_wt + (size_t)i * 1048576, dec_self_b + i * 2048, true, x_dec);
-    LN(x_dec, dec_ln_g + i * 1536 + 512, dec_ln_b + i * 1536 + 512, hbuf);
-    cross_attn(dec_cross_wt + (size_t)i * 1048576, dec_cross_b + i * 2048, x_dec);
-    ffn_block(x_dec, dec_f1t + (size_t)i * 1048576, dec_ffn_b1 + i * 2048,
-              dec_f2t + (size_t)i * 1048576, dec_ffn_b2 + i * 512,
-              dec_ln_g + i * 1536 + 1024, dec_ln_b + i * 1536 + 1024);
-  }
-  LN(x_dec, dec_norm_g, dec_norm_b, hbuf);
-
-  k_proj256<<<dim3(125, 8), 512, 0, stream>>>(hbuf, proj_wt, logits, proj_b);
+  a.tj.ofs[8] = acc;
+  a.ntile = acc;
+
+  hipMemsetAsync(barmem, 0, 512, stream);
+  k_mega<<<dim3(kGrid), dim3(256), 0, stream>>>(a);
+  k_proj256<<<dim3(125, 8), 512, 0, stream>>>(a.hbuf, proj_wt, logits, proj_b);
   k_lsm_bf<<<kM, 640, 0, stream>>>(logits, (float*)d_out);
 }
```

Result: slower. 2.256 ms (+210.5%).
